# Kernel tuning notes

Hardware: AMD Instinct MI355X
Metric: run time of the kernel (lower is better)

## Reference

```python
import jax, jax.numpy as jnp
import numpy as np
from jax import lax

B, A, ACT, ID, FEAT, HID, NA = 4096, 20, 21, 20, 32, 64, 21
VIEW = 5 * 7 * 6  # 210
NB = A * (1 + ACT)  # 440


def setup_inputs() -> dict:
    key = jax.random.key(0)
    ks = jax.random.split(key, 16)
    view = jax.random.normal(ks[0], (B, VIEW), dtype=jnp.float32)
    feat = jax.random.normal(ks[1], (B, FEAT), dtype=jnp.float32)
    # neighbor ids in [-2, ID): -2 => absent (skipped), -1 => self, >=0 => neighbor index
    ids = jax.random.randint(ks[2], (B, A), -2, ID).astype(jnp.float32)
    act_idx = jax.random.randint(ks[3], (B, A), 0, ACT)
    acts = jax.nn.one_hot(act_idx, ACT, dtype=jnp.float32)
    zero_act = jax.random.uniform(ks[4], (B, A)) < 0.3
    acts = jnp.where(zero_act[..., None], 0.0, acts)
    nb = jnp.concatenate([ids[..., None], acts], axis=-1).reshape(B, NB)
    obs = jnp.concatenate([view, feat, nb], axis=1)  # [B, 682]
    s = 0.05
    return {
        'obs': obs,
        'conv1_w': jax.random.normal(ks[5], (32, 5, 3, 3), jnp.float32) * s,
        'conv1_b': jax.random.normal(ks[6], (32,), jnp.float32) * s,
        'conv2_w': jax.random.normal(ks[7], (32, 32, 3, 3), jnp.float32) * s,
        'conv2_b': jax.random.normal(ks[8], (32,), jnp.float32) * s,
        'fc1_w': jax.random.normal(ks[9], (192, HID), jnp.float32) * s,
        'fc1_b': jax.random.normal(ks[10], (HID,), jnp.float32) * s,
        'fc2_w': jax.random.normal(ks[11], (HID + FEAT + ID + ACT, HID), jnp.float32) * s,
        'fc2_b': jax.random.normal(ks[12], (HID,), jnp.float32) * s,
        'fc3_w': jax.random.normal(ks[13], (HID, NA), jnp.float32) * s,
        'fc3_b': jax.random.normal(ks[14], (NA,), jnp.float32) * s,
    }


def reference(obs, conv1_w, conv1_b, conv2_w, conv2_b, fc1_w, fc1_b, fc2_w, fc2_b, fc3_w, fc3_b):
    view = obs[:, :VIEW].reshape(-1, 5, 7, 6)
    feat = obs[:, VIEW:VIEW + FEAT]
    nb = obs[:, -NB:].reshape(-1, A, 1 + ACT)
    ids = nb[..., 0]          # [B, A] float ids
    acts = nb[..., 1:]        # [B, A, ACT]

    dn = ('NCHW', 'OIHW', 'NCHW')
    o = jax.nn.relu(lax.conv_general_dilated(view, conv1_w, (1, 1), 'VALID', dimension_numbers=dn)
                    + conv1_b[None, :, None, None])
    o = jax.nn.relu(lax.conv_general_dilated(o, conv2_w, (1, 1), 'VALID', dimension_numbers=dn)
                    + conv2_b[None, :, None, None])          # [B, 32, 3, 2]
    x = jax.nn.relu(o.reshape(-1, 192) @ fc1_w + fc1_b)      # [B, HID]

    # fc2 is linear in the concat(x, feat, id_onehot, act); split its weight accordingly.
    W2x = fc2_w[:HID]
    W2f = fc2_w[HID:HID + FEAT]
    W2id = fc2_w[HID + FEAT:HID + FEAT + ID]
    W2act = fc2_w[HID + FEAT + ID:]

    id_int = ids.astype(jnp.int32)
    # self (id==-1) uses zeros for the id one-hot; one_hot gives zeros for negatives.
    idvec = jax.nn.one_hot(id_int, ID, dtype=obs.dtype)       # [B, A, ID]

    base = x @ W2x + feat @ W2f + fc2_b                        # [B, HID]
    idterm = jnp.einsum('bai,ih->bah', idvec, W2id)            # [B, A, HID]
    actterm = jnp.einsum('baj,jh->bah', acts, W2act)           # [B, A, HID]

    # single-row case (self or known neighbor action)
    h_s = jax.nn.relu(base[:, None, :] + idterm + actterm)     # [B, A, HID]
    q_s = h_s @ fc3_w + fc3_b                                  # [B, A, NA]

    # expand case: unknown action => enumerate all ACT one-hot actions and sum q
    h_e = jax.nn.relu(base[:, None, None, :] + idterm[:, :, None, :] + W2act[None, None, :, :])  # [B, A, ACT, HID]
    q_e = (h_e @ fc3_w + fc3_b).sum(axis=2)                    # [B, A, NA]

    valid = id_int >= -1
    act_zero = jnp.all(acts == 0.0, axis=-1)
    expand = valid & (id_int >= 0) & act_zero

    q_agent = jnp.where(expand[..., None], q_e, q_s)
    q_agent = jnp.where(valid[..., None], q_agent, 0.0)
    return q_agent.sum(axis=1)                                 # [B, NA]
```

## Files before the change

kernel.cpp:

```cpp
#include <hip/hip_runtime.h>

typedef __attribute__((ext_vector_type(8))) short bf16x8;
typedef __attribute__((ext_vector_type(4))) float f32x4;

constexpr int OBS  = 682;
constexpr int ACTN = 21;
constexpr int MB   = 8;

constexpr int WS_C1U  = 0;
constexpr int WS_C2U  = 2048;
constexpr int WS_F1U  = 11264;
constexpr int WS_TOTU = 23552;

__device__ __forceinline__ unsigned short f2bf(float x) {
    unsigned u = __float_as_uint(x);
    return (unsigned short)((u + 0x7FFFu + ((u >> 16) & 1u)) >> 16);
}

__global__ void repack_b(const float* __restrict__ c1w, const float* __restrict__ c2w,
                         const float* __restrict__ f1w, unsigned short* __restrict__ wsu) {
    int i = blockIdx.x * 256 + threadIdx.x;
    if (i >= WS_TOTU) return;
    int frag = i >> 9, within = i & 511;
    int l = within >> 3, j = within & 7;
    int q = l >> 4, l15 = l & 15;
    float v = 0.f;
    if (frag < 4) {
        int s = frag >> 1, nt = frag & 1;
        int k = 32 * s + 8 * q + j, n = 16 * nt + l15;
        if (k < 45) v = c1w[n * 45 + k];
    } else if (frag < 22) {
        int f = frag - 4, s = f >> 1, nt = f & 1;
        int k = 32 * s + 8 * q + j, n = 16 * nt + l15;
        v = c2w[n * 288 + k];
    } else {
        int f = frag - 22, s = f >> 2, nt = f & 3;
        int k = 32 * s + 8 * q + j, n = 16 * nt + l15;
        v = f1w[k * 64 + n];
    }
    wsu[i] = f2bf(v);
}

__global__ __launch_bounds__(512, 6) void mfma_k(
    const float* __restrict__ obs,
    const float* __restrict__ c1b, const float* __restrict__ c2b,
    const float* __restrict__ f1b, const float* __restrict__ f2w,
    const float* __restrict__ f2b, const float* __restrict__ f3w,
    const float* __restrict__ f3b,
    const unsigned short* __restrict__ wsu,
    float* __restrict__ out)
{
    const int t = threadIdx.x;
    const int w = t >> 6, l = t & 63;
    const int q = l >> 4, l15 = l & 15;
    const int b8 = blockIdx.x * MB;

    __shared__ __align__(16) unsigned short sv[MB * 280];
    __shared__ __align__(16) unsigned short uA[7680];
    __shared__ __align__(16) unsigned short sc1[MB * 640];
    __shared__ __align__(16) float sfeat32[MB * 32];
    __shared__ __align__(16) float sx32[MB * 64];
    __shared__ __align__(16) float sW[2624];
    __shared__ __align__(16) float sbias[224];
    __shared__ int smeta[MB * 20];
    __shared__ unsigned short tap1[48], tap2[288], mb2[MB * 6];

    unsigned short* sc2 = sc1;
    float* sh32 = sx32;

    for (int e = t; e < MB * 210; e += 512) {
        int row = e / 210, i2 = e - row * 210;
        int c = i2 / 42, rem = i2 - c * 42;
        int r3 = rem / 6, col = rem - r3 * 6;
        sv[row * 280 + c * 56 + r3 * 8 + col] = f2bf(obs[(long)(b8 + row) * OBS + i2]);
    }
    if (t < MB * 32) {
        int row = t >> 5, j = t & 31;
        sfeat32[t] = obs[(long)(b8 + row) * OBS + 210 + j];
    }
    {
        const float4* srcw = (const float4*)(f2w + 96 * 64);
        float4* dw = (float4*)sW;
        if (t < 512) { dw[t] = srcw[t]; if (t < 144) dw[512 + t] = srcw[512 + t]; }
    }
    if (t < 224) {
        float v = 0.f;
        if (t < 32) v = c1b[t];
        else if (t < 64) v = c2b[t - 32];
        else if (t < 128) v = f1b[t - 64];
        else if (t < 192) v = f2b[t - 128];
        else if (t < 213) v = f3b[t - 192];
        sbias[t] = v;
    }
    if (t < 48) {
        int c = t / 9, rem = t - c * 9;
        tap1[t] = (unsigned short)(c * 56 + (rem / 3) * 8 + (rem % 3));
    }
    if (t < 288) {
        int ic = t / 9, rem = t - ic * 9;
        tap2[t] = (unsigned short)(ic * 20 + (rem / 3) * 4 + (rem % 3));
    }
    if (t < MB * 6) {
        int row = t / 6, pos = t - row * 6;
        mb2[t] = (unsigned short)(row * 640 + (pos >> 1) * 4 + (pos & 1));
    }
    if (t < MB * 20) {
        int row = t / 20, a = t - row * 20;
        const float* nb = obs + (long)(b8 + row) * OBS + 242 + a * 22;
        int id = (int)nb[0];
        int js = -1;
        #pragma unroll
        for (int j = 0; j < ACTN; ++j) {
            float av = nb[1 + j];
            js = (av != 0.f && js < 0) ? j : js;
        }
        int mode = (id < -1) ? 0 : ((id >= 0 && js < 0) ? 1 : 2);
        smeta[t] = ((id + 2) << 8) | (mode << 5) | (js + 1);
    }
    __syncthreads();

    for (int e = t; e < 160 * 45; e += 512) {
        int rowm = e / 45, k = e - rowm * 45;
        int brow = rowm / 20, pos = rowm - brow * 20;
        int base = brow * 280 + (pos >> 2) * 8 + (pos & 3);
        uA[rowm * 48 + k] = sv[base + tap1[k]];
    }
    if (t < 480) {
        int rowm = t / 3, k = 45 + (t % 3);
        uA[rowm * 48 + k] = 0;
    }
    __syncthreads();

    {
        #pragma unroll
        for (int u = 0; u < 3; ++u) {
            int p = w + 8 * u;
            if (p < 20) {
                int mt = p >> 1, nt = p & 1;
                f32x4 acc = {0.f, 0.f, 0.f, 0.f};
                {
                    bf16x8 a = *(const bf16x8*)&uA[(mt * 16 + l15) * 48 + 8 * q];
                    bf16x8 bb = *(const bf16x8*)&wsu[WS_C1U + (0 + nt) * 512 + l * 8];
                    acc = __builtin_amdgcn_mfma_f32_16x16x32_bf16(a, bb, acc, 0, 0, 0);
                }
                {
                    bf16x8 a = {0, 0, 0, 0, 0, 0, 0, 0};
                    if (q < 2) a = *(const bf16x8*)&uA[(mt * 16 + l15) * 48 + 32 + 8 * q];
                    bf16x8 bb = *(const bf16x8*)&wsu[WS_C1U + (2 + nt) * 512 + l * 8];
                    acc = __builtin_amdgcn_mfma_f32_16x16x32_bf16(a, bb, acc, 0, 0, 0);
                }
                int oc = nt * 16 + l15;
                float bias = sbias[oc];
                #pragma unroll
                for (int r = 0; r < 4; ++r) {
                    int m = mt * 16 + 4 * q + r;
                    int row = m / 20, pos = m - row * 20;
                    sc1[row * 640 + oc * 20 + pos] = f2bf(fmaxf(acc[r] + bias, 0.f));
                }
            }
        }
    }
    __syncthreads();

    for (int e = t; e < 48 * 160; e += 512) {
        int m = e / 160, k = e - m * 160;
        uA[m * 160 + k] = sc1[mb2[m] + tap2[k]];
    }
    __syncthreads();

    f32x4 c2acc = {0.f, 0.f, 0.f, 0.f};
    const bool c2act = (w < 6);
    const int c2mt = w >> 1, c2nt = w & 1;
    if (c2act) {
        #pragma unroll
        for (int s = 0; s < 5; ++s) {
            bf16x8 a = *(const bf16x8*)&uA[(c2mt * 16 + l15) * 160 + 32 * s + 8 * q];
            bf16x8 bb = *(const bf16x8*)&wsu[WS_C2U + (s * 2 + c2nt) * 512 + l * 8];
            c2acc = __builtin_amdgcn_mfma_f32_16x16x32_bf16(a, bb, c2acc, 0, 0, 0);
        }
    }
    __syncthreads();

    for (int e = t; e < 48 * 128; e += 512) {
        int m = e >> 7, k2 = e & 127;
        uA[m * 160 + k2] = sc1[mb2[m] + tap2[160 + k2]];
    }
    __syncthreads();

    if (c2act) {
        #pragma unroll
        for (int s = 5; s < 9; ++s) {
            bf16x8 a = *(const bf16x8*)&uA[(c2mt * 16 + l15) * 160 + 32 * (s - 5) + 8 * q];
            bf16x8 bb = *(const bf16x8*)&wsu[WS_C2U + (s * 2 + c2nt) * 512 + l * 8];
            c2acc = __builtin_amdgcn_mfma_f32_16x16x32_bf16(a, bb, c2acc, 0, 0, 0);
        }
        int oc = c2nt * 16 + l15;
        float bias = sbias[32 + oc];
        #pragma unroll
        for (int r = 0; r < 4; ++r) {
            int m = c2mt * 16 + 4 * q + r;
            int row = m / 6, pos = m - row * 6;
            sc2[row * 200 + oc * 6 + pos] = f2bf(fmaxf(c2acc[r] + bias, 0.f));
        }
    }
    __syncthreads();

    if (w < 4) {
        int nt = w;
        f32x4 acc = {0.f, 0.f, 0.f, 0.f};
        #pragma unroll
        for (int s = 0; s < 6; ++s) {
            bf16x8 a = *(const bf16x8*)&sc2[l15 * 200 + 32 * s + 8 * q];
            bf16x8 bb = *(const bf16x8*)&wsu[WS_F1U + (s * 4 + nt) * 512 + l * 8];
            acc = __builtin_amdgcn_mfma_f32_16x16x32_bf16(a, bb, acc, 0, 0, 0);
        }
        int h = nt * 16 + l15;
        float bias = sbias[64 + h];
        #pragma unroll
        for (int r = 0; r < 4; ++r) {
            int row = 4 * q + r;
            if (row < MB) sx32[row * 64 + h] = fmaxf(acc[r] + bias, 0.f);
        }
    }
    __syncthreads();

    float cnt;
    {
        const int row = w;
        float a0 = sbias[128 + l], a1 = 0.f;
        #pragma unroll 4
        for (int k = 0; k < 64; k += 2) {
            a0 = fmaf(sx32[row * 64 + k],     f2w[(k    ) * 64 + l], a0);
            a1 = fmaf(sx32[row * 64 + k + 1], f2w[(k + 1) * 64 + l], a1);
        }
        #pragma unroll 4
        for (int k = 0; k < 32; k += 2) {
            a0 = fmaf(sfeat32[row * 32 + k],     f2w[(64 + k    ) * 64 + l], a0);
            a1 = fmaf(sfeat32[row * 32 + k + 1], f2w[(64 + k + 1) * 64 + l], a1);
        }
        const float base_l = a0 + a1;
        float hacc = 0.f;
        cnt = 0.f;
        for (int a = 0; a < 20; ++a) {
            int m = smeta[row * 20 + a];
            int mode = (m >> 5) & 3;
            if (mode == 0) continue;
            int id = (m >> 8) - 2;
            int js = (m & 31) - 1;
            float u = base_l + ((id >= 0) ? sW[id * 64 + l] : 0.f);
            if (mode == 1) {
                float h0 = 0.f, h1 = 0.f, h2 = 0.f;
                #pragma unroll
                for (int j = 0; j < ACTN; j += 3) {
                    h0 += fmaxf(u + sW[1280 + (j    ) * 64 + l], 0.f);
                    h1 += fmaxf(u + sW[1280 + (j + 1) * 64 + l], 0.f);
                    h2 += fmaxf(u + sW[1280 + (j + 2) * 64 + l], 0.f);
                }
                hacc += (h0 + h1) + h2;
                cnt  += 21.f;
            } else {
                float ar = (js >= 0) ? sW[1280 + js * 64 + l] : 0.f;
                hacc += fmaxf(u + ar, 0.f);
                cnt  += 1.f;
            }
        }
        sh32[row * 64 + l] = hacc;
    }

    if (l < ACTN) {
        float qv = cnt * sbias[192 + l];
        float q1 = 0.f;
        #pragma unroll 4
        for (int h = 0; h < 64; h += 2) {
            qv = fmaf(sh32[w * 64 + h],     f3w[(h    ) * 21 + l], qv);
            q1 = fmaf(sh32[w * 64 + h + 1], f3w[(h + 1) * 21 + l], q1);
        }
        out[(long)(b8 + w) * 21 + l] = qv + q1;
    }
}

__device__ __forceinline__ float comp4(float4 v, int i) {
    return (i == 0) ? v.x : (i == 1) ? v.y : (i == 2) ? v.z : v.w;
}

constexpr int S_V = 0, S_OBS = 280, S_C1 = 968, S_PART = 1608, S_C2 = 1992,
              S_X = 2184, S_H = 2248, S_TOT = 2312;

__global__ __launch_bounds__(64, 4) void fallback_k(
    const float* __restrict__ obs,
    const float* __restrict__ c1w, const float* __restrict__ c1b,
    const float* __restrict__ c2w, const float* __restrict__ c2b,
    const float* __restrict__ f1w, const float* __restrict__ f1b,
    const float* __restrict__ f2w, const float* __restrict__ f2b,
    const float* __restrict__ f3w, const float* __restrict__ f3b,
    float* __restrict__ out)
{
    const int b = blockIdx.x, t = threadIdx.x;
    __shared__ __align__(16) float sb[S_TOT];
    __shared__ int s_meta[20];
    {
        const float* orow = obs + (long)b * OBS;
        #pragma unroll
        for (int k = 0; k < 4; ++k) {
            int i = t + k * 64;
            if (i < 210) {
                int c = i / 42, rem = i - 42 * c, r = rem / 6, col = rem - 6 * r;
                sb[S_V + c * 56 + r * 8 + col] = orow[i];
            }
        }
        #pragma unroll
        for (int k = 0; k < 8; ++k) {
            int i = 210 + t + k * 64;
            if (i < OBS) sb[S_OBS + i] = orow[i];
        }
    }
    __syncthreads();
    if (t < 20) {
        const float* nb = &sb[S_OBS + 242 + t * 22];
        int id = (int)nb[0], js = -1;
        #pragma unroll
        for (int j = 0; j < ACTN; ++j) {
            float av = nb[1 + j];
            js = (av != 0.f && js < 0) ? j : js;
        }
        int mode = (id < -1) ? 0 : ((id >= 0 && js < 0) ? 1 : 2);
        s_meta[t] = ((id + 2) << 8) | (mode << 5) | (js + 1);
    }
    {
        const int oc = t & 31, s = t >> 5;
        float acc[12];
        #pragma unroll
        for (int i = 0; i < 12; ++i) acc[i] = 0.f;
        #pragma unroll
        for (int c = 0; c < 5; ++c) {
            float wv[9];
            #pragma unroll
            for (int k = 0; k < 9; ++k) wv[k] = c1w[oc * 45 + c * 9 + k];
            #pragma unroll
            for (int rr = 0; rr < 5; ++rr) {
                const float* rowp = &sb[S_V + c * 56 + (2 * s + rr) * 8];
                float4 v0 = *(const float4*)rowp;
                float2 v1 = *(const float2*)(rowp + 4);
                float c0 = v0.x, c1 = v0.y, c2 = v0.z, c3 = v0.w, c4 = v1.x, c5 = v1.y;
                #pragma unroll
                for (int kh = 0; kh < 3; ++kh) {
                    int ohl = rr - kh;
                    if (ohl < 0 || ohl > 2) continue;
                    acc[ohl*4+0] = fmaf(c0, wv[kh*3+0], acc[ohl*4+0]);
                    acc[ohl*4+0] = fmaf(c1, wv[kh*3+1], acc[ohl*4+0]);
                    acc[ohl*4+0] = fmaf(c2, wv[kh*3+2], acc[ohl*4+0]);
                    acc[ohl*4+1] = fmaf(c1, wv[kh*3+0], acc[ohl*4+1]);
                    acc[ohl*4+1] = fmaf(c2, wv[kh*3+1], acc[ohl*4+1]);
                    acc[ohl*4+1] = fmaf(c3, wv[kh*3+2], acc[ohl*4+1]);
                    acc[ohl*4+2] = fmaf(c2, wv[kh*3+0], acc[ohl*4+2]);
                    acc[ohl*4+2] = fmaf(c3, wv[kh*3+1], acc[ohl*4+2]);
                    acc[ohl*4+2] = fmaf(c4, wv[kh*3+2], acc[ohl*4+2]);
                    acc[ohl*4+3] = fmaf(c3, wv[kh*3+0], acc[ohl*4+3]);
                    acc[ohl*4+3] = fmaf(c4, wv[kh*3+1], acc[ohl*4+3]);
                    acc[ohl*4+3] = fmaf(c5, wv[kh*3+2], acc[ohl*4+3]);
                }
            }
        }
        float bias = c1b[oc];
        #pragma unroll
        for (int ohl = 0; ohl < 3; ++ohl) {
            int oh = 2 * s + ohl;
            float4 o4 = make_float4(fmaxf(acc[ohl*4+0] + bias, 0.f), fmaxf(acc[ohl*4+1] + bias, 0.f),
                                    fmaxf(acc[ohl*4+2] + bias, 0.f), fmaxf(acc[ohl*4+3] + bias, 0.f));
            *(float4*)&sb[S_C1 + oc * 20 + oh * 4] = o4;
        }
    }
    __syncthreads();
    {
        const int oc = t & 31, half = t >> 5;
        float a0=0,a1=0,a2=0,a3=0,a4=0,a5=0;
        #pragma unroll 4
        for (int icc = 0; icc < 16; ++icc) {
            const int ic = half * 16 + icc;
            const float4* rp = (const float4*)&sb[S_C1 + ic * 20];
            float4 r0 = rp[0], r1 = rp[1], r2 = rp[2], r3 = rp[3], r4 = rp[4];
            float wv[9];
            #pragma unroll
            for (int k = 0; k < 9; ++k) wv[k] = c2w[oc * 288 + ic * 9 + k];
            #pragma unroll
            for (int kh = 0; kh < 3; ++kh) {
                float4 ra = (kh == 0) ? r0 : (kh == 1) ? r1 : r2;
                float4 rb = (kh == 0) ? r1 : (kh == 1) ? r2 : r3;
                float4 rc = (kh == 0) ? r2 : (kh == 1) ? r3 : r4;
                #pragma unroll
                for (int kw = 0; kw < 3; ++kw) {
                    float ww = wv[kh * 3 + kw];
                    a0 = fmaf(comp4(ra, kw),     ww, a0);
                    a1 = fmaf(comp4(ra, kw + 1), ww, a1);
                    a2 = fmaf(comp4(rb, kw),     ww, a2);
                    a3 = fmaf(comp4(rb, kw + 1), ww, a3);
                    a4 = fmaf(comp4(rc, kw),     ww, a4);
                    a5 = fmaf(comp4(rc, kw + 1), ww, a5);
                }
            }
        }
        float* pp = &sb[S_PART + (half * 32 + oc) * 6];
        pp[0]=a0; pp[1]=a1; pp[2]=a2; pp[3]=a3; pp[4]=a4; pp[5]=a5;
    }
    __syncthreads();
    if (t < 32) {
        float bias = c2b[t];
        #pragma unroll
        for (int p = 0; p < 6; ++p)
            sb[S_C2 + t * 6 + p] = fmaxf(sb[S_PART + t * 6 + p] + sb[S_PART + (32 + t) * 6 + p] + bias, 0.f);
    }
    __syncthreads();
    {
        float a0 = f1b[t], a1 = 0.f;
        const float4* xp = (const float4*)&sb[S_C2];
        #pragma unroll 4
        for (int kq = 0; kq < 48; ++kq) {
            float4 x = xp[kq];
            a0 = fmaf(x.x, f1w[(4*kq+0)*64+t], a0);
            a1 = fmaf(x.y, f1w[(4*kq+1)*64+t], a1);
            a0 = fmaf(x.z, f1w[(4*kq+2)*64+t], a0);
            a1 = fmaf(x.w, f1w[(4*kq+3)*64+t], a1);
        }
        sb[S_X + t] = fmaxf(a0 + a1, 0.f);
    }
    __syncthreads();
    float base_t;
    {
        float a0 = f2b[t], a1 = 0.f;
        const float4* xp = (const float4*)&sb[S_X];
        #pragma unroll 4
        for (int kq = 0; kq < 16; ++kq) {
            float4 x = xp[kq];
            a0 = fmaf(x.x, f2w[(4*kq+0)*64+t], a0);
            a1 = fmaf(x.y, f2w[(4*kq+1)*64+t], a1);
            a0 = fmaf(x.z, f2w[(4*kq+2)*64+t], a0);
            a1 = fmaf(x.w, f2w[(4*kq+3)*64+t], a1);
        }
        const float2* fp = (const float2*)&sb[S_OBS + 210];
        #pragma unroll 4
        for (int i2 = 0; i2 < 16; ++i2) {
            float2 v = fp[i2];
            a0 = fmaf(v.x, f2w[(64 + i2*2+0)*64+t], a0);
            a1 = fmaf(v.y, f2w[(64 + i2*2+1)*64+t], a1);
        }
        base_t = a0 + a1;
    }
    const float* W2id = f2w + 96 * 64;
    const float* W2act = f2w + 116 * 64;
    float hacc = 0.f, cnt = 0.f;
    for (int a = 0; a < 20; ++a) {
        int m = s_meta[a];
        int mode = (m >> 5) & 3;
        if (mode == 0) continue;
        int id = (m >> 8) - 2, js = (m & 31) - 1;
        float u = base_t + ((id >= 0) ? W2id[id * 64 + t] : 0.f);
        if (mode == 1) {
            float h0=0,h1=0,h2=0;
            #pragma unroll
            for (int j = 0; j < ACTN; j += 3) {
                h0 += fmaxf(u + W2act[(j    )*64+t], 0.f);
                h1 += fmaxf(u + W2act[(j + 1)*64+t], 0.f);
                h2 += fmaxf(u + W2act[(j + 2)*64+t], 0.f);
            }
            hacc += (h0 + h1) + h2; cnt += 21.f;
        } else {
            float ar = (js >= 0) ? W2act[js * 64 + t] : 0.f;
            hacc += fmaxf(u + ar, 0.f); cnt += 1.f;
        }
    }
    sb[S_H + t] = hacc;
    __syncthreads();
    if (t < ACTN) {
        float q0 = cnt * f3b[t], q1 = 0.f;
        const float4* hp = (const float4*)&sb[S_H];
        #pragma unroll 4
        for (int h4 = 0; h4 < 16; ++h4) {
            float4 v = hp[h4];
            q0 = fmaf(v.x, f3w[(h4*4+0)*21+t], q0);
            q1 = fmaf(v.y, f3w[(h4*4+1)*21+t], q1);
            q0 = fmaf(v.z, f3w[(h4*4+2)*21+t], q0);
            q1 = fmaf(v.w, f3w[(h4*4+3)*21+t], q1);
        }
        out[b * 21 + t] = q0 + q1;
    }
}

extern "C" void kernel_launch(void* const* d_in, const int* in_sizes, int n_in,
                              void* d_out, int out_size, void* d_ws, size_t ws_size,
                              hipStream_t stream) {
    const float* obs = (const float*)d_in[0];
    const float* c1w = (const float*)d_in[1];
    const float* c1b = (const float*)d_in[2];
    const float* c2w = (const float*)d_in[3];
    const float* c2b = (const float*)d_in[4];
    const float* f1w = (const float*)d_in[5];
    const float* f1b = (const float*)d_in[6];
    const float* f2w = (const float*)d_in[7];
    const float* f2b = (const float*)d_in[8];
    const float* f3w = (const float*)d_in[9];
    const float* f3b = (const float*)d_in[10];
    float* o = (float*)d_out;
    const int B = in_sizes[0] / OBS;

    if (ws_size >= (size_t)WS_TOTU * 2 && (B % MB) == 0) {
        unsigned short* wsu = (unsigned short*)d_ws;
        repack_b<<<(WS_TOTU + 255) / 256, 256, 0, stream>>>(c1w, c2w, f1w, wsu);
        mfma_k<<<B / MB, 512, 0, stream>>>(obs, c1b, c2b, f1b, f2w, f2b, f3w, f3b, wsu, o);
    } else {
        fallback_k<<<B, 64, 0, stream>>>(obs, c1w, c1b, c2w, c2b, f1w, f1b,
                                         f2w, f2b, f3w, f3b, o);
    }
}
```

Before: 28.93 us.

## Gather conv im2col operands directly into MFMA registers, drop staging buffer

Removes the shared im2col staging buffer (uA) for both conv layers. Each lane now builds its bf16x8 A-fragment by gathering from the source activations through tap-offset tables. This cuts the separate im2col passes and four block-wide barriers. Conv2 runs all nine K-steps in one loop, and sc1 gets a padded stride of 648 with its own sc2 buffer. In exchange, each lane does eight scalar LDS gathers per MFMA instead of one vector load, and the gathers may hit bank conflicts.

```diff
diff --git a/kernel.cpp b/kernel.cpp
--- a/kernel.cpp
+++ b/kernel.cpp
@@ -41,6 +41,8 @@
     wsu[i] = f2bf(v);
 }
 
+constexpr int SC1S = 648;
+
 __global__ __launch_bounds__(512, 6) void mfma_k(
     const float* __restrict__ obs,
     const float* __restrict__ c1b, const float* __restrict__ c2b,
@@ -56,16 +58,16 @@
     const int b8 = blockIdx.x * MB;
 
     __shared__ __align__(16) unsigned short sv[MB * 280];
-    __shared__ __align__(16) unsigned short uA[7680];
-    __shared__ __align__(16) unsigned short sc1[MB * 640];
+    __shared__ __align__(16) unsigned short sc1[MB * SC1S];
+    __shared__ __align__(16) unsigned short sc2[MB * 200];
     __shared__ __align__(16) float sfeat32[MB * 32];
     __shared__ __align__(16) float sx32[MB * 64];
     __shared__ __align__(16) float sW[2624];
     __shared__ __align__(16) float sbias[224];
     __shared__ int smeta[MB * 20];
-    __shared__ unsigned short tap1[48], tap2[288], mb2[MB * 6];
-
-    unsigned short* sc2 = sc1;
+    __shared__ __align__(16) unsigned short tap1[48];
+    __shared__ __align__(16) unsigned short tap2[288];
+
     float* sh32 = sx32;
 
     for (int e = t; e < MB * 210; e += 512) {
@@ -94,15 +96,12 @@
     }
     if (t < 48) {
         int c = t / 9, rem = t - c * 9;
-        tap1[t] = (unsigned short)(c * 56 + (rem / 3) * 8 + (rem % 3));
+        tap1[t] = (t < 45) ? (unsigned short)(c * 56 + (rem / 3) * 8 + (rem % 3))
+                           : (unsigned short)0;
     }
     if (t < 288) {
         int ic = t / 9, rem = t - ic * 9;
         tap2[t] = (unsigned short)(ic * 20 + (rem / 3) * 4 + (rem % 3));
-    }
-    if (t < MB * 6) {
-        int row = t / 6, pos = t - row * 6;
-        mb2[t] = (unsigned short)(row * 640 + (pos >> 1) * 4 + (pos & 1));
     }
     if (t < MB * 20) {
         int row = t / 20, a = t - row * 20;
@@ -119,33 +118,35 @@
     }
     __syncthreads();
 
-    for (int e = t; e < 160 * 45; e += 512) {
-        int rowm = e / 45, k = e - rowm * 45;
-        int brow = rowm / 20, pos = rowm - brow * 20;
-        int base = brow * 280 + (pos >> 2) * 8 + (pos & 3);
-        uA[rowm * 48 + k] = sv[base + tap1[k]];
-    }
-    if (t < 480) {
-        int rowm = t / 3, k = 45 + (t % 3);
-        uA[rowm * 48 + k] = 0;
-    }
-    __syncthreads();
-
     {
         #pragma unroll
         for (int u = 0; u < 3; ++u) {
             int p = w + 8 * u;
             if (p < 20) {
                 int mt = p >> 1, nt = p & 1;
+                int m = mt * 16 + l15;
+                int brow = m / 20, pos = m - brow * 20;
+                int base1 = brow * 280 + ((pos >> 2) << 3) + (pos & 3);
                 f32x4 acc = {0.f, 0.f, 0.f, 0.f};
                 {
-                    bf16x8 a = *(const bf16x8*)&uA[(mt * 16 + l15) * 48 + 8 * q];
+                    const unsigned short* tp = &tap1[8 * q];
+                    bf16x8 a;
+                    #pragma unroll
+                    for (int j = 0; j < 8; ++j)
+                        a[j] = (short)sv[base1 + tp[j]];
                     bf16x8 bb = *(const bf16x8*)&wsu[WS_C1U + (0 + nt) * 512 + l * 8];
                     acc = __builtin_amdgcn_mfma_f32_16x16x32_bf16(a, bb, acc, 0, 0, 0);
                 }
                 {
                     bf16x8 a = {0, 0, 0, 0, 0, 0, 0, 0};
-                    if (q < 2) a = *(const bf16x8*)&uA[(mt * 16 + l15) * 48 + 32 + 8 * q];
+                    if (q < 2) {
+                        const unsigned short* tp = &tap1[32 + 8 * q];
+                        #pragma unroll
+                        for (int j = 0; j < 8; ++j) {
+                            unsigned short v = sv[base1 + tp[j]];
+                            a[j] = (8 * q + j < 13) ? (short)v : (short)0;
+                        }
+                    }
                     bf16x8 bb = *(const bf16x8*)&wsu[WS_C1U + (2 + nt) * 512 + l * 8];
                     acc = __builtin_amdgcn_mfma_f32_16x16x32_bf16(a, bb, acc, 0, 0, 0);
                 }
@@ -153,54 +154,38 @@
                 float bias = sbias[oc];
                 #pragma unroll
                 for (int r = 0; r < 4; ++r) {
-                    int m = mt * 16 + 4 * q + r;
-                    int row = m / 20, pos = m - row * 20;
-                    sc1[row * 640 + oc * 20 + pos] = f2bf(fmaxf(acc[r] + bias, 0.f));
-                }
-            }
-        }
-    }
-    __syncthreads();
-
-    for (int e = t; e < 48 * 160; e += 512) {
-        int m = e / 160, k = e - m * 160;
-        uA[m * 160 + k] = sc1[mb2[m] + tap2[k]];
-    }
-    __syncthreads();
-
-    f32x4 c2acc = {0.f, 0.f, 0.f, 0.f};
-    const bool c2act = (w < 6);
-    const int c2mt = w >> 1, c2nt = w & 1;
-    if (c2act) {
-        #pragma unroll
-        for (int s = 0; s < 5; ++s) {
-            bf16x8 a = *(const bf16x8*)&uA[(c2mt * 16 + l15) * 160 + 32 * s + 8 * q];
-            bf16x8 bb = *(const bf16x8*)&wsu[WS_C2U + (s * 2 + c2nt) * 512 + l * 8];
-            c2acc = __builtin_amdgcn_mfma_f32_16x16x32_bf16(a, bb, c2acc, 0, 0, 0);
-        }
-    }
-    __syncthreads();
-
-    for (int e = t; e < 48 * 128; e += 512) {
-        int m = e >> 7, k2 = e & 127;
-        uA[m * 160 + k2] = sc1[mb2[m] + tap2[160 + k2]];
-    }
-    __syncthreads();
-
-    if (c2act) {
-        #pragma unroll
-        for (int s = 5; s < 9; ++s) {
-            bf16x8 a = *(const bf16x8*)&uA[(c2mt * 16 + l15) * 160 + 32 * (s - 5) + 8 * q];
-            bf16x8 bb = *(const bf16x8*)&wsu[WS_C2U + (s * 2 + c2nt) * 512 + l * 8];
-            c2acc = __builtin_amdgcn_mfma_f32_16x16x32_bf16(a, bb, c2acc, 0, 0, 0);
-        }
-        int oc = c2nt * 16 + l15;
+                    int mm = mt * 16 + 4 * q + r;
+                    int row = mm / 20, ps = mm - row * 20;
+                    sc1[row * SC1S + oc * 20 + ps] = f2bf(fmaxf(acc[r] + bias, 0.f));
+                }
+            }
+        }
+    }
+    __syncthreads();
+
+    if (w < 6) {
+        int mt = w >> 1, nt = w & 1;
+        int m = mt * 16 + l15;
+        int rowm = m / 6, posm = m - rowm * 6;
+        int base2 = rowm * SC1S + ((posm >> 1) << 2) + (posm & 1);
+        f32x4 acc = {0.f, 0.f, 0.f, 0.f};
+        #pragma unroll
+        for (int s = 0; s < 9; ++s) {
+            const unsigned short* tp = &tap2[32 * s + 8 * q];
+            bf16x8 a;
+            #pragma unroll
+            for (int j = 0; j < 8; ++j)
+                a[j] = (short)sc1[base2 + tp[j]];
+            bf16x8 bb = *(const bf16x8*)&wsu[WS_C2U + (s * 2 + nt) * 512 + l * 8];
+            acc = __builtin_amdgcn_mfma_f32_16x16x32_bf16(a, bb, acc, 0, 0, 0);
+        }
+        int oc = nt * 16 + l15;
         float bias = sbias[32 + oc];
         #pragma unroll
         for (int r = 0; r < 4; ++r) {
-            int m = c2mt * 16 + 4 * q + r;
-            int row = m / 6, pos = m - row * 6;
-            sc2[row * 200 + oc * 6 + pos] = f2bf(fmaxf(c2acc[r] + bias, 0.f));
+            int mm = mt * 16 + 4 * q + r;
+            int row = mm / 6, ps = mm - row * 6;
+            sc2[row * 200 + oc * 6 + ps] = f2bf(fmaxf(acc[r] + bias, 0.f));
         }
     }
     __syncthreads();
```

Result: faster. 26.97 us (-6.8%).
